# Kernel optimization log

Hardware: AMD Instinct MI355X
Metric: run time of the kernel (lower is better)

## Reference

```python
import jax, jax.numpy as jnp
import numpy as np

B, C, FS, Z_DIM, OUT_C, F_SIZE = 256, 512, 16, 64, 1, 3
NZ = FS * FS  # 256


def setup_inputs() -> dict:
    key = jax.random.key(0)
    k1, k2, k3, k4, k5 = jax.random.split(key, 5)
    # z: [B, C, H, W]
    z = jax.random.normal(k1, (B, C, FS, FS), dtype=jnp.float32)
    # 512 independent per-channel Linear(Nz -> z_dim): stacked weights/biases
    lim_in = 1.0 / np.sqrt(NZ)
    W_in = jax.random.uniform(k2, (C, NZ, Z_DIM), minval=-lim_in, maxval=lim_in, dtype=jnp.float32)
    b_in = jax.random.uniform(k3, (C, Z_DIM), minval=-lim_in, maxval=lim_in, dtype=jnp.float32)
    # shared Linear(z_dim -> out_channels*f_size*f_size)
    lim_out = 1.0 / np.sqrt(Z_DIM)
    W_out = jax.random.uniform(k4, (Z_DIM, OUT_C * F_SIZE * F_SIZE), minval=-lim_out, maxval=lim_out, dtype=jnp.float32)
    b_out = jax.random.uniform(k5, (OUT_C * F_SIZE * F_SIZE,), minval=-lim_out, maxval=lim_out, dtype=jnp.float32)
    return {"z": z, "W_in": W_in, "b_in": b_in, "W_out": W_out, "b_out": b_out}


def reference(z, W_in, b_in, W_out, b_out):
    batch = z.shape[0]
    # flatten each channel's HxW map: [B, C, Nz]
    x = z.reshape(batch, C, NZ)
    # per-channel Linear as one batched GEMM: [B, C, z_dim]
    a = jnp.einsum('bcn,cnz->bcz', x, W_in) + b_in[None, :, :]
    # shared output Linear: [B, C, out_c*f*f]
    k = jnp.einsum('bcz,zk->bck', a, W_out) + b_out
    # [B, C, out_channels, f_size, f_size]
    return k.reshape(batch, C, OUT_C, F_SIZE, F_SIZE)
```

## Files before the change

kernel.cpp:

```cpp
#include <hip/hip_runtime.h>

#define BB 256
#define CC 512
#define NZ 256
#define ZD 64
#define KK 9

template<int CTRL>
__device__ __forceinline__ float dpp_add(float v) {
    int o = __builtin_amdgcn_update_dpp(0, __float_as_int(v), CTRL, 0xF, 0xF, true);
    return v + __int_as_float(o);
}
__device__ __forceinline__ float red8(float v) {
    v = dpp_add<0xB1>(v);
    v = dpp_add<0x4E>(v);
    v = dpp_add<0x141>(v);
    return v;
}

__global__ __launch_bounds__(512, 2)
void hyper_kernel(const float* __restrict__ z,
                  const float* __restrict__ W_in,
                  const float* __restrict__ b_in,
                  const float* __restrict__ W_out,
                  const float* __restrict__ b_out,
                  float* __restrict__ out) {
    __shared__ __align__(16) float s_wfT[KK * NZ];
    __shared__ __align__(16) float s_woutT[KK * ZD];
    __shared__ float s_bin[ZD];
    __shared__ float s_biask[KK];

    const int c = blockIdx.x;
    const int t = threadIdx.x;

    for (int i = t; i < KK * ZD; i += 512) {
        float v = W_out[i];
        int zz = i / KK, k = i - zz * KK;
        s_woutT[k * ZD + zz] = v;
    }
    if (t < ZD) s_bin[t] = b_in[c * ZD + t];
    __syncthreads();

    {
        const int n = t >> 1, half = t & 1;
        const float* wrow = W_in + ((size_t)c * NZ + n) * ZD + half * 32;
        float acc[KK];
#pragma unroll
        for (int k = 0; k < KK; ++k) acc[k] = 0.f;
#pragma unroll
        for (int j = 0; j < 8; ++j) {
            const float4 w = *reinterpret_cast<const float4*>(wrow + 4 * j);
#pragma unroll
            for (int k = 0; k < KK; ++k) {
                const float4 wo = *reinterpret_cast<const float4*>(
                    &s_woutT[k * ZD + half * 32 + 4 * j]);
                acc[k] += w.x * wo.x + w.y * wo.y + w.z * wo.z + w.w * wo.w;
            }
        }
#pragma unroll
        for (int k = 0; k < KK; ++k) acc[k] = dpp_add<0xB1>(acc[k]);
        if (half == 0) {
#pragma unroll
            for (int k = 0; k < KK; ++k) s_wfT[k * NZ + n] = acc[k];
        }
        if (t < KK) {
            float s = 0.f;
            for (int zz = 0; zz < ZD; ++zz) s += s_bin[zz] * s_woutT[t * ZD + zz];
            s_biask[t] = s + b_out[t];
        }
    }
    __syncthreads();

    const int lane = t & 63;
    const int wave = t >> 6;
    const int g = lane >> 3;
    const int sub = lane & 7;
    const int b0 = wave * 32 + g * 4;
    const float biasS = s_biask[sub];
    const float bias8 = s_biask[8];

    const float* xp = z + ((size_t)b0 * CC + c) * NZ + sub * 4;
    const size_t bstr = (size_t)CC * NZ;

    float acc[4][KK];
#pragma unroll
    for (int bb = 0; bb < 4; ++bb)
#pragma unroll
        for (int k = 0; k < KK; ++k) acc[bb][k] = 0.f;

    float4 xb[2][4];
#pragma unroll
    for (int bb = 0; bb < 4; ++bb)
        xb[0][bb] = *reinterpret_cast<const float4*>(xp + bb * bstr);

#pragma unroll
    for (int j = 0; j < 8; ++j) {
        if (j < 7) {
#pragma unroll
            for (int bb = 0; bb < 4; ++bb)
                xb[(j + 1) & 1][bb] =
                    *reinterpret_cast<const float4*>(xp + bb * bstr + (j + 1) * 32);
        }
#pragma unroll
        for (int k = 0; k < KK; ++k) {
            const float4 wf = *reinterpret_cast<const float4*>(
                &s_wfT[k * NZ + sub * 4 + j * 32]);
#pragma unroll
            for (int bb = 0; bb < 4; ++bb) {
                const float4 x = xb[j & 1][bb];
                acc[bb][k] += x.x * wf.x + x.y * wf.y + x.z * wf.z + x.w * wf.w;
            }
        }
    }

#pragma unroll
    for (int bb = 0; bb < 4; ++bb)
#pragma unroll
        for (int k = 0; k < KK; ++k) acc[bb][k] = red8(acc[bb][k]);

#pragma unroll
    for (int bb = 0; bb < 4; ++bb) {
        float v = acc[bb][0];
#pragma unroll
        for (int k = 1; k < 8; ++k) {
            if (sub == k) v = acc[bb][k];
        }
        const size_t o0 = ((size_t)(b0 + bb) * CC + c) * KK;
        out[o0 + sub] = v + biasS;
        if (sub == 0) out[o0 + 8] = acc[bb][8] + bias8;
    }
}

extern "C" void kernel_launch(void* const* d_in, const int* in_sizes, int n_in,
                              void* d_out, int out_size, void* d_ws, size_t ws_size,
                              hipStream_t stream) {
    const float* z     = (const float*)d_in[0];
    const float* W_in  = (const float*)d_in[1];
    const float* b_in  = (const float*)d_in[2];
    const float* W_out = (const float*)d_in[3];
    const float* b_out = (const float*)d_in[4];
    float* out = (float*)d_out;
    hyper_kernel<<<dim3(CC), dim3(512), 0, stream>>>(z, W_in, b_in, W_out, b_out, out);
}
```

Measured before the change: 227.6 us.

## Split into weight-folding and output kernels with channel-by-batch tiling

Splits the fused kernel into two launches. The first folds W_in with W_out per channel into a workspace, along with a folded bias. The second tiles 4 channels by 64 batches per block, stages outputs in shared memory so stores are coalesced float4 writes, and deepens the z prefetch to three stages. This targets the scattered 9-float output writes and the long serial per-block batch loop. The cost is a second launch, a workspace round-trip through global memory, and the folded weights being re-read by four batch tiles.

```diff
diff --git a/kernel.cpp b/kernel.cpp
--- a/kernel.cpp
+++ b/kernel.cpp
@@ -5,6 +5,9 @@
 #define NZ 256
 #define ZD 64
 #define KK 9
+#define WFSZ (KK * NZ)
+#define CT 4
+#define BT 64
 
 template<int CTRL>
 __device__ __forceinline__ float dpp_add(float v) {
@@ -19,17 +22,11 @@
 }
 
 __global__ __launch_bounds__(512, 2)
-void hyper_kernel(const float* __restrict__ z,
-                  const float* __restrict__ W_in,
-                  const float* __restrict__ b_in,
-                  const float* __restrict__ W_out,
-                  const float* __restrict__ b_out,
-                  float* __restrict__ out) {
-    __shared__ __align__(16) float s_wfT[KK * NZ];
+void wf_kernel(const float* __restrict__ W_in, const float* __restrict__ b_in,
+               const float* __restrict__ W_out, const float* __restrict__ b_out,
+               float* __restrict__ wf, float* __restrict__ biask) {
     __shared__ __align__(16) float s_woutT[KK * ZD];
     __shared__ float s_bin[ZD];
-    __shared__ float s_biask[KK];
-
     const int c = blockIdx.x;
     const int t = threadIdx.x;
 
@@ -41,46 +38,69 @@
     if (t < ZD) s_bin[t] = b_in[c * ZD + t];
     __syncthreads();
 
-    {
-        const int n = t >> 1, half = t & 1;
-        const float* wrow = W_in + ((size_t)c * NZ + n) * ZD + half * 32;
-        float acc[KK];
+    const int n = t >> 1, half = t & 1;
+    const float* wrow = W_in + ((size_t)c * NZ + n) * ZD + half * 32;
+    float acc[KK];
 #pragma unroll
-        for (int k = 0; k < KK; ++k) acc[k] = 0.f;
+    for (int k = 0; k < KK; ++k) acc[k] = 0.f;
 #pragma unroll
-        for (int j = 0; j < 8; ++j) {
-            const float4 w = *reinterpret_cast<const float4*>(wrow + 4 * j);
+    for (int j = 0; j < 8; ++j) {
+        const float4 w = *reinterpret_cast<const float4*>(wrow + 4 * j);
 #pragma unroll
-            for (int k = 0; k < KK; ++k) {
-                const float4 wo = *reinterpret_cast<const float4*>(
-                    &s_woutT[k * ZD + half * 32 + 4 * j]);
-                acc[k] += w.x * wo.x + w.y * wo.y + w.z * wo.z + w.w * wo.w;
-            }
-        }
-#pragma unroll
-        for (int k = 0; k < KK; ++k) acc[k] = dpp_add<0xB1>(acc[k]);
-        if (half == 0) {
-#pragma unroll
-            for (int k = 0; k < KK; ++k) s_wfT[k * NZ + n] = acc[k];
-        }
-        if (t < KK) {
-            float s = 0.f;
-            for (int zz = 0; zz < ZD; ++zz) s += s_bin[zz] * s_woutT[t * ZD + zz];
-            s_biask[t] = s + b_out[t];
+        for (int k = 0; k < KK; ++k) {
+            const float4 wo = *reinterpret_cast<const float4*>(
+                &s_woutT[k * ZD + half * 32 + 4 * j]);
+            acc[k] += w.x * wo.x + w.y * wo.y + w.z * wo.z + w.w * wo.w;
         }
     }
+#pragma unroll
+    for (int k = 0; k < KK; ++k) acc[k] = dpp_add<0xB1>(acc[k]);
+    if (half == 0) {
+#pragma unroll
+        for (int k = 0; k < KK; ++k)
+            wf[(size_t)c * WFSZ + k * NZ + n] = acc[k];
+    }
+    if (t < KK) {
+        float s = 0.f;
+        for (int zz = 0; zz < ZD; ++zz) s += s_bin[zz] * s_woutT[t * ZD + zz];
+        biask[c * KK + t] = s + b_out[t];
+    }
+}
+
+__global__ __launch_bounds__(512, 4)
+void out_kernel(const float* __restrict__ z, const float* __restrict__ wf,
+                const float* __restrict__ biask, float* __restrict__ out) {
+    __shared__ __align__(16) float s_wf[CT * WFSZ];
+    __shared__ __align__(16) float s_out[BT * CT * KK];
+    __shared__ float s_b[CT * KK];
+
+    const int ctile = blockIdx.x & 127;
+    const int btile = blockIdx.x >> 7;
+    const int c0 = ctile * CT;
+    const int b0 = btile * BT;
+    const int t = threadIdx.x;
+    const int G64 = t >> 3;
+    const int sub = t & 7;
+    const int c_idx = G64 & 3;
+    const int bq = G64 >> 2;
+
+    const size_t zrow = (size_t)CC * NZ;
+    const float* zp = z + ((size_t)(b0 + bq * 4) * CC + (c0 + c_idx)) * NZ + sub * 4;
+    float4 xb[3][4];
+#pragma unroll
+    for (int bb = 0; bb < 4; ++bb)
+        xb[0][bb] = *reinterpret_cast<const float4*>(zp + bb * zrow);
+#pragma unroll
+    for (int bb = 0; bb < 4; ++bb)
+        xb[1][bb] = *reinterpret_cast<const float4*>(zp + bb * zrow + 32);
+
+    {
+        const float4* g4 = reinterpret_cast<const float4*>(wf + (size_t)c0 * WFSZ);
+        float4* s4 = reinterpret_cast<float4*>(s_wf);
+        for (int i = t; i < CT * (WFSZ / 4); i += 512) s4[i] = g4[i];
+        if (t < CT * KK) s_b[t] = biask[c0 * KK + t];
+    }
     __syncthreads();
-
-    const int lane = t & 63;
-    const int wave = t >> 6;
-    const int g = lane >> 3;
-    const int sub = lane & 7;
-    const int b0 = wave * 32 + g * 4;
-    const float biasS = s_biask[sub];
-    const float bias8 = s_biask[8];
-
-    const float* xp = z + ((size_t)b0 * CC + c) * NZ + sub * 4;
-    const size_t bstr = (size_t)CC * NZ;
 
     float acc[4][KK];
 #pragma unroll
@@ -88,27 +108,23 @@
 #pragma unroll
         for (int k = 0; k < KK; ++k) acc[bb][k] = 0.f;
 
-    float4 xb[2][4];
-#pragma unroll
-    for (int bb = 0; bb < 4; ++bb)
-        xb[0][bb] = *reinterpret_cast<const float4*>(xp + bb * bstr);
+    const float* wbase = &s_wf[c_idx * WFSZ + sub * 4];
 
 #pragma unroll
     for (int j = 0; j < 8; ++j) {
-        if (j < 7) {
+        if (j + 2 < 8) {
 #pragma unroll
             for (int bb = 0; bb < 4; ++bb)
-                xb[(j + 1) & 1][bb] =
-                    *reinterpret_cast<const float4*>(xp + bb * bstr + (j + 1) * 32);
+                xb[(j + 2) % 3][bb] =
+                    *reinterpret_cast<const float4*>(zp + bb * zrow + (j + 2) * 32);
         }
 #pragma unroll
         for (int k = 0; k < KK; ++k) {
-            const float4 wf = *reinterpret_cast<const float4*>(
-                &s_wfT[k * NZ + sub * 4 + j * 32]);
+            const float4 w = *reinterpret_cast<const float4*>(wbase + k * NZ + j * 32);
 #pragma unroll
             for (int bb = 0; bb < 4; ++bb) {
-                const float4 x = xb[j & 1][bb];
-                acc[bb][k] += x.x * wf.x + x.y * wf.y + x.z * wf.z + x.w * wf.w;
+                const float4 x = xb[j % 3][bb];
+                acc[bb][k] += x.x * w.x + x.y * w.y + x.z * w.z + x.w * w.w;
             }
         }
     }
@@ -118,6 +134,8 @@
 #pragma unroll
         for (int k = 0; k < KK; ++k) acc[bb][k] = red8(acc[bb][k]);
 
+    const float biasS = s_b[c_idx * KK + sub];
+    const float bias8 = s_b[c_idx * KK + 8];
 #pragma unroll
     for (int bb = 0; bb < 4; ++bb) {
         float v = acc[bb][0];
@@ -125,9 +143,17 @@
         for (int k = 1; k < 8; ++k) {
             if (sub == k) v = acc[bb][k];
         }
-        const size_t o0 = ((size_t)(b0 + bb) * CC + c) * KK;
-        out[o0 + sub] = v + biasS;
-        if (sub == 0) out[o0 + 8] = acc[bb][8] + bias8;
+        const int bl = bq * 4 + bb;
+        s_out[bl * (CT * KK) + c_idx * KK + sub] = v + biasS;
+        if (sub == 0) s_out[bl * (CT * KK) + c_idx * KK + 8] = acc[bb][8] + bias8;
+    }
+    __syncthreads();
+
+    for (int i = t; i < BT * KK; i += 512) {
+        const int bl = i / KK, q = i - bl * KK;
+        const size_t dst = ((size_t)(b0 + bl) * CC + c0) * KK + q * 4;
+        *reinterpret_cast<float4*>(&out[dst]) =
+            *reinterpret_cast<const float4*>(&s_out[bl * (CT * KK) + q * 4]);
     }
 }
 
@@ -140,5 +166,10 @@
     const float* W_out = (const float*)d_in[3];
     const float* b_out = (const float*)d_in[4];
     float* out = (float*)d_out;
-    hyper_kernel<<<dim3(CC), dim3(512), 0, stream>>>(z, W_in, b_in, W_out, b_out, out);
+
+    float* wfbuf = (float*)d_ws;
+    float* biask = (float*)d_ws + (size_t)CC * WFSZ;
+
+    wf_kernel<<<dim3(CC), dim3(512), 0, stream>>>(W_in, b_in, W_out, b_out, wfbuf, biask);
+    out_kernel<<<dim3(4 * 128), dim3(512), 0, stream>>>(z, wfbuf, biask, out);
 }
```

Result: no change. 229.9 us (+1.0%).
